# Kernel tuning notes

Hardware: AMD Instinct MI355X
Metric: run time of the kernel (lower is better)

Reference implementation:

```python
import math
import jax, jax.numpy as jnp
import numpy as np

B, T, C, H, V = 2, 512, 768, 12, 50304
HD = C // H
EPS_LN = 1e-5
SINK_ITERS = 6           # MAX_ITER_SINK
N_STEPS = 20             # ceil((1-0)/h_max), h_max=0.05
H_STEP = 1.0 / N_STEPS   # Euler step size h


def layer_norm(x, w, b):
    mu = jnp.mean(x, axis=-1, keepdims=True)
    var = jnp.mean(jnp.square(x - mu), axis=-1, keepdims=True)
    return (x - mu) * jax.lax.rsqrt(var + EPS_LN) * w + b


def sinkhorn_pi(Cmat):
    # log-domain Sinkhorn (eps=1) on cost matrix Cmat [N, T, T]; returns transport plan pi
    n = Cmat.shape[-1]
    log_marg = -jnp.log(jnp.asarray(n, Cmat.dtype))  # log(1/n), uniform marginals
    u = jnp.zeros(Cmat.shape[:-1], Cmat.dtype)
    v = jnp.zeros(Cmat.shape[:-1], Cmat.dtype)
    def M(u, v):
        return -Cmat + u[..., :, None] + v[..., None, :]
    for _ in range(SINK_ITERS):
        u = (log_marg - jax.nn.logsumexp(M(u, v), axis=-1)) + u
        v = (log_marg - jax.nn.logsumexp(M(u, v), axis=-2)) + v
    return jnp.exp(M(u, v))


def block_f(z, t, attn_ln_w, attn_ln_b, c_attn_w, c_attn_b, c_proj_w, c_proj_b,
            mlp_ln_w, mlp_ln_b, c_fc_w, c_fc_b, mlp_proj_w, mlp_proj_b):
    Bz, Tz, Cz = z.shape
    tcol = jnp.full((Bz, Tz, 1), t, z.dtype)
    # attention sub-block: LN over C+1 dims (x concat time)
    x = layer_norm(jnp.concatenate([z, tcol], axis=-1), attn_ln_w, attn_ln_b)
    qkv = x @ c_attn_w + c_attn_b                      # [B,T,3C]
    q, k, v = jnp.split(qkv, 3, axis=-1)
    q = q.reshape(Bz, Tz, H, HD).transpose(0, 2, 1, 3)  # [B,H,T,hd]
    k = k.reshape(Bz, Tz, H, HD).transpose(0, 2, 1, 3)
    v = v.reshape(Bz, Tz, H, HD).transpose(0, 2, 1, 3)
    att = jnp.einsum('bhqd,bhkd->bhqk', q, k) * (1.0 / math.sqrt(HD))
    mask = jnp.tril(jnp.ones((Tz, Tz), dtype=bool))
    att = jax.nn.softmax(jnp.where(mask, att, -jnp.inf), axis=-1)
    pi = sinkhorn_pi(att.reshape(Bz * H, Tz, Tz)) * Tz  # sink(att)[0] * n
    y = jnp.einsum('bhqk,bhkd->bhqd', pi.reshape(Bz, H, Tz, Tz), v)
    y = y.transpose(0, 2, 1, 3).reshape(Bz, Tz, Cz)
    y = y @ c_proj_w + c_proj_b
    # MLP sub-block on LN(concat(attn_out, t))
    ht = layer_norm(jnp.concatenate([y, tcol], axis=-1), mlp_ln_w, mlp_ln_b)
    h1 = jax.nn.gelu(ht @ c_fc_w + c_fc_b, approximate=False)
    return h1 @ mlp_proj_w + mlp_proj_b


def setup_inputs() -> dict:
    key = jax.random.key(0)
    ks = jax.random.split(key, 8)
    s = 0.02
    return {
        'idx': jax.random.randint(ks[0], (B, T), 0, V),
        'wte': s * jax.random.normal(ks[1], (V, C), jnp.float32),
        'wpe': s * jax.random.normal(ks[2], (T, C), jnp.float32),
        'attn_ln_w': jnp.ones((C + 1,), jnp.float32),
        'attn_ln_b': jnp.zeros((C + 1,), jnp.float32),
        'c_attn_w': s * jax.random.normal(ks[3], (C + 1, 3 * C), jnp.float32),
        'c_attn_b': jnp.zeros((3 * C,), jnp.float32),
        'c_proj_w': s * jax.random.normal(ks[4], (C, C), jnp.float32),
        'c_proj_b': jnp.zeros((C,), jnp.float32),
        'mlp_ln_w': jnp.ones((C + 1,), jnp.float32),
        'mlp_ln_b': jnp.zeros((C + 1,), jnp.float32),
        'c_fc_w': s * jax.random.normal(ks[5], (C + 1, 4 * C), jnp.float32),
        'c_fc_b': jnp.zeros((4 * C,), jnp.float32),
        'mlp_proj_w': s * jax.random.normal(ks[6], (4 * C, C), jnp.float32),
        'mlp_proj_b': jnp.zeros((C,), jnp.float32),
        'lnf_w': jnp.ones((C,), jnp.float32),
        'lnf_b': jnp.zeros((C,), jnp.float32),
    }


def reference(idx, wte, wpe, attn_ln_w, attn_ln_b, c_attn_w, c_attn_b, c_proj_w,
              c_proj_b, mlp_ln_w, mlp_ln_b, c_fc_w, c_fc_b, mlp_proj_w, mlp_proj_b,
              lnf_w, lnf_b):
    x = wte[idx] + wpe[jnp.arange(idx.shape[1])]  # [B,T,C]

    def step(carry, _):
        z, t = carry
        dz = block_f(z, t, attn_ln_w, attn_ln_b, c_attn_w, c_attn_b, c_proj_w,
                     c_proj_b, mlp_ln_w, mlp_ln_b, c_fc_w, c_fc_b, mlp_proj_w,
                     mlp_proj_b)
        return (z + H_STEP * dz, t + H_STEP), None

    (x, _), _ = jax.lax.scan(step, (x, jnp.float32(0.0)), None, length=N_STEPS)
    x = layer_norm(x, lnf_w, lnf_b)
    logits = x[:, -1:, :] @ wte.T  # inference path: last position only, tied head
    return logits
```

## Files before the change

### kernel.cpp

```cpp
#include <hip/hip_runtime.h>
#include <hip/hip_bf16.h>
#include <math.h>

typedef unsigned short ushortT;
typedef unsigned int uintT;

#define Bc   2
#define Tc   512
#define Cc   768
#define Hc   12
#define HDc  64
#define Vc   50304
#define BTc  (Bc*Tc)
#define NHc  (Bc*Hc)
#define C3   (3*Cc)
#define C4   (4*Cc)
#define EPS_LN 1e-5f
#define H_STEP 0.05f
#define INVN (1.0f/512.0f)
#define SB   4

typedef float f32x4 __attribute__((ext_vector_type(4)));
typedef __bf16 bf16x8 __attribute__((ext_vector_type(8)));
typedef ushortT us8 __attribute__((ext_vector_type(8)));
typedef uintT u32x4 __attribute__((ext_vector_type(4)));

__device__ __forceinline__ ushortT f2bf(float f) {
    union { float f; unsigned u; } x; x.f = f;
    unsigned r = (x.u + 0x7fffu + ((x.u >> 16) & 1u)) >> 16;
    return (ushortT)r;
}
__device__ __forceinline__ float bf2f(ushortT b) {
    union { unsigned u; float f; } x; x.u = ((unsigned)b) << 16;
    return x.f;
}
__device__ __forceinline__ float bflo(uintT w) {
    union { unsigned u; float f; } x; x.u = w << 16;
    return x.f;
}
__device__ __forceinline__ float bfhi(uintT w) {
    union { unsigned u; float f; } x; x.u = w & 0xffff0000u;
    return x.f;
}

__device__ __forceinline__ void gll16(const ushortT* g, ushortT* l) {
    __builtin_amdgcn_global_load_lds(
        (const __attribute__((address_space(1))) unsigned int*)g,
        (__attribute__((address_space(3))) unsigned int*)l,
        16, 0, 0);
}

__device__ __forceinline__ float waveReduceSumX(float v) {
    for (int o = 32; o; o >>= 1) v += __shfl_xor(v, o);
    return v;
}
__device__ __forceinline__ float blockReduceSum(float v) {
    __shared__ float sm[4];
    for (int o = 32; o; o >>= 1) v += __shfl_down(v, o);
    __syncthreads();
    if ((threadIdx.x & 63) == 0) sm[threadIdx.x >> 6] = v;
    __syncthreads();
    return sm[0] + sm[1] + sm[2] + sm[3];
}

__global__ __launch_bounds__(256)
void wtrans_kernel(const float* __restrict__ W, ushortT* __restrict__ out,
                   int K, int N)
{
    __shared__ float t[32][33];
    int k0 = blockIdx.x * 32, n0 = blockIdx.y * 32;
    int tx = threadIdx.x & 31, ty = threadIdx.x >> 5;
    for (int r = ty; r < 32; r += 8)
        t[r][tx] = W[(size_t)(k0 + r) * N + n0 + tx];
    __syncthreads();
    for (int r = ty; r < 32; r += 8)
        out[(size_t)(n0 + r) * K + k0 + tx] = f2bf(t[tx][r]);
}

__global__ __launch_bounds__(256)
void embed_ln(const int* __restrict__ idx, const float* __restrict__ wte,
              const float* __restrict__ wpe, float* __restrict__ z,
              const float* __restrict__ lnw, const float* __restrict__ lnb,
              ushortT* __restrict__ xlnb, float* __restrict__ xt)
{
    int row = blockIdx.x, tid = threadIdx.x;
    int tok = idx[row];
    float v[3];
#pragma unroll
    for (int q = 0; q < 3; ++q) {
        int c = tid + 256 * q;
        float val = wte[(size_t)tok * Cc + c] + wpe[(size_t)(row & (Tc - 1)) * Cc + c];
        z[(size_t)row * Cc + c] = val;
        v[q] = val;
    }
    float s = blockReduceSum(v[0] + v[1] + v[2]);
    float mu = s / 769.f;
    float d0 = v[0] - mu, d1 = v[1] - mu, d2 = v[2] - mu;
    float ss = blockReduceSum(d0 * d0 + d1 * d1 + d2 * d2);
    float dt = 0.f - mu;
    float var = (ss + dt * dt) / 769.f;
    float rs = rsqrtf(var + EPS_LN);
#pragma unroll
    for (int q = 0; q < 3; ++q) {
        int c = tid + 256 * q;
        xlnb[(size_t)row * Cc + c] = f2bf((v[q] - mu) * rs * lnw[c] + lnb[c]);
    }
    if (tid == 0) xt[row] = dt * rs * lnw[Cc] + lnb[Cc];
}

__global__ __launch_bounds__(256)
void ln_kernel(const float* __restrict__ X, const float* __restrict__ w,
               const float* __restrict__ bb, void* __restrict__ Y,
               float* __restrict__ yt, int hasT, float tval,
               int rowMul, int rowAdd, int obf16)
{
    int orow = blockIdx.x;
    int r = orow * rowMul + rowAdd;
    const float* x = X + (size_t)r * Cc;
    int tid = threadIdx.x;
    float xv[3];
#pragma unroll
    for (int q = 0; q < 3; ++q) xv[q] = x[tid + 256 * q];
    float s = blockReduceSum(xv[0] + xv[1] + xv[2]);
    float cnt = hasT ? 769.f : 768.f;
    float mu = (s + (hasT ? tval : 0.f)) / cnt;
    float d0 = xv[0] - mu, d1 = xv[1] - mu, d2 = xv[2] - mu;
    float ss = blockReduceSum(d0 * d0 + d1 * d1 + d2 * d2);
    float dt = tval - mu;
    float var = (ss + (hasT ? dt * dt : 0.f)) / cnt;
    float rs = rsqrtf(var + EPS_LN);
#pragma unroll
    for (int q = 0; q < 3; ++q) {
        int c = tid + 256 * q;
        float v = (xv[q] - mu) * rs * w[c] + bb[c];
        if (obf16) ((ushortT*)Y)[(size_t)orow * Cc + c] = f2bf(v);
        else       ((float*)Y)[(size_t)orow * Cc + c] = v;
    }
    if (hasT && tid == 0) yt[orow] = dt * rs * w[Cc] + bb[Cc];
}

template <int EPI>
__global__ __launch_bounds__(256)
void gemm_bt(const ushortT* __restrict__ A, int lda,
             const ushortT* __restrict__ Bt, int ldb,
             void* __restrict__ Cm, int ldc, int K,
             const float* __restrict__ bias,
             const float* __restrict__ extraA,
             const float* __restrict__ extraB)
{
    __shared__ __align__(16) ushortT Als[128][32];
    __shared__ __align__(16) ushortT Bls[128][32];
    if (EPI == 4) {
        int koff = blockIdx.z * K;
        A += koff; Bt += koff;
    }
    int tid = threadIdx.x;
    int lane = tid & 63, wid = tid >> 6;
    int wm = wid >> 1, wn = wid & 1;
    int m0 = blockIdx.y * 128, n0 = blockIdx.x * 128;
    f32x4 acc[4][4];
    const f32x4 fz = {0.f, 0.f, 0.f, 0.f};
#pragma unroll
    for (int i = 0; i < 4; ++i)
#pragma unroll
        for (int j = 0; j < 4; ++j) acc[i][j] = fz;

    for (int k0 = 0; k0 < K; k0 += 32) {
#pragma unroll
        for (int is = 0; is < 2; ++is) {
            int ch = is * 256 + tid;
            int m = ch >> 2, kc = ch & 3;
            gll16(A + (size_t)(m0 + m) * lda + k0 + kc * 8, &Als[0][0] + ch * 8);
            gll16(Bt + (size_t)(n0 + m) * ldb + k0 + kc * 8, &Bls[0][0] + ch * 8);
        }
        __syncthreads();
        bf16x8 af[4], bfv[4];
#pragma unroll
        for (int i = 0; i < 4; ++i) {
            int row = wm * 64 + i * 16 + (lane & 15);
            af[i] = *(const bf16x8*)&Als[row][(lane >> 4) * 8];
            int col = wn * 64 + i * 16 + (lane & 15);
            bfv[i] = *(const bf16x8*)&Bls[col][(lane >> 4) * 8];
        }
#pragma unroll
        for (int i = 0; i < 4; ++i)
#pragma unroll
            for (int j = 0; j < 4; ++j)
                acc[i][j] = __builtin_amdgcn_mfma_f32_16x16x32_bf16(af[i], bfv[j], acc[i][j], 0, 0, 0);
        __syncthreads();
    }
#pragma unroll
    for (int i = 0; i < 4; ++i) {
#pragma unroll
        for (int j = 0; j < 4; ++j) {
#pragma unroll
            for (int r = 0; r < 4; ++r) {
                int row = m0 + wm * 64 + i * 16 + (lane >> 4) * 4 + r;
                int col = n0 + wn * 64 + j * 16 + (lane & 15);
                float v = acc[i][j][r];
                if (extraA) v += extraA[row] * extraB[col];
                if (bias) v += bias[col];
                size_t oi = (size_t)row * ldc + col;
                if (EPI == 0) {
                    ((ushortT*)Cm)[oi] = f2bf(v);
                } else if (EPI == 1) {
                    v = 0.5f * v * (1.f + erff(v * 0.70710678118654752440f));
                    ((ushortT*)Cm)[oi] = f2bf(v);
                } else if (EPI == 3) {
                    ((float*)Cm)[oi] = v;
                } else if (EPI == 4) {
                    ((float*)Cm)[(size_t)blockIdx.z * ((size_t)BTc * Cc) + oi] = v;
                }
            }
        }
    }
}

__global__ __launch_bounds__(512)
void sinkfused(const ushortT* __restrict__ qkvb, ushortT* __restrict__ E,
               float* __restrict__ avec, ushortT* __restrict__ vTs,
               float* __restrict__ partials, unsigned* __restrict__ ctr,
               unsigned barBase)
{
    int gb = blockIdx.x;
    int n = gb >> 2, r = gb & 3;
    int row0 = r * 128;
    int b = n / Hc, h = n - b * Hc;
    int tid = threadIdx.x;
    int l = tid & 63, w = tid >> 6;
    __shared__ __align__(16) ushortT Els[128][Tc];
    __shared__ __align__(16) ushortT Kls[128][64];
    __shared__ float a_s[128];
    __shared__ float b_s[Tc];
    ushortT* Eg = E + (size_t)n * Tc * Tc;
    const f32x4 fz = {0.f, 0.f, 0.f, 0.f};

    int qrow = b * Tc + row0 + w * 16 + (l & 15);
    const ushortT* qp = qkvb + (size_t)qrow * C3 + h * HDc + (l >> 4) * 8;
    bf16x8 aq0 = *(const bf16x8*)(qp);
    bf16x8 aq1 = *(const bf16x8*)(qp + 32);

    int kcmax = r + 1;
    f32x4 acc[32];
#pragma unroll
    for (int j = 0; j < 32; ++j) acc[j] = fz;

#pragma unroll
    for (int kc = 0; kc < 4; ++kc) {
        if (kc < kcmax) {
            {
                int ch = tid;
                int row = ch >> 3, c16 = (ch & 7) ^ (row & 7);
                gll16(qkvb + (size_t)(b * Tc + kc * 128 + row) * C3 + Cc + h * HDc + c16 * 8,
                      &Kls[0][0] + ch * 8);
                ch = tid + 512;
                row = ch >> 3; c16 = (ch & 7) ^ (row & 7);
                gll16(qkvb + (size_t)(b * Tc + kc * 128 + row) * C3 + Cc + h * HDc + c16 * 8,
                      &Kls[0][0] + ch * 8);
            }
            __syncthreads();
#pragma unroll
            for (int jj = 0; jj < 8; ++jj) {
                int krow = jj * 16 + (l & 15);
                int c16a = (l >> 4);
                int c16b = 4 + (l >> 4);
                bf16x8 bk0 = *(const bf16x8*)(&Kls[0][0] + ((size_t)krow * 8 + (c16a ^ (krow & 7))) * 8);
                bf16x8 bk1 = *(const bf16x8*)(&Kls[0][0] + ((size_t)krow * 8 + (c16b ^ (krow & 7))) * 8);
                acc[kc * 8 + jj] = __builtin_amdgcn_mfma_f32_16x16x32_bf16(aq0, bk0, acc[kc * 8 + jj], 0, 0, 0);
                acc[kc * 8 + jj] = __builtin_amdgcn_mfma_f32_16x16x32_bf16(aq1, bk1, acc[kc * 8 + jj], 0, 0, 0);
            }
            __syncthreads();
        }
    }

    int nvalid = kcmax * 8;
    int colbase = (l & 15);
    int rowa[4];
#pragma unroll
    for (int e = 0; e < 4; ++e) rowa[e] = row0 + w * 16 + (l >> 4) * 4 + e;

    float mx[4] = {-INFINITY, -INFINITY, -INFINITY, -INFINITY};
#pragma unroll
    for (int j = 0; j < 32; ++j) {
        if (j < nvalid) {
            int col = j * 16 + colbase;
#pragma unroll
            for (int e = 0; e < 4; ++e)
                if (col <= rowa[e]) mx[e] = fmaxf(mx[e], acc[j][e] * 0.125f);
        }
    }
#pragma unroll
    for (int e = 0; e < 4; ++e)
        for (int o = 1; o < 16; o <<= 1) mx[e] = fmaxf(mx[e], __shfl_xor(mx[e], o));

    float se[4] = {0.f, 0.f, 0.f, 0.f};
#pragma unroll
    for (int j = 0; j < 32; ++j) {
        if (j < nvalid) {
            int col = j * 16 + colbase;
#pragma unroll
            for (int e = 0; e < 4; ++e) {
                float exv = (col <= rowa[e]) ? __expf(acc[j][e] * 0.125f - mx[e]) : 0.f;
                acc[j][e] = exv;
                se[e] += exv;
            }
        }
    }
#pragma unroll
    for (int e = 0; e < 4; ++e)
        for (int o = 1; o < 16; o <<= 1) se[e] += __shfl_xor(se[e], o);
    float inv[4];
#pragma unroll
    for (int e = 0; e < 4; ++e) inv[e] = 1.f / se[e];

    float rsum[4] = {0.f, 0.f, 0.f, 0.f};
#pragma unroll
    for (int j = 0; j < 32; ++j) {
        if (j < nvalid) {
            int col = j * 16 + colbase;
#pragma unroll
            for (int e = 0; e < 4; ++e) {
                float Ee = __expf(-(acc[j][e] * inv[e]));
                rsum[e] += Ee;
                Els[w * 16 + (l >> 4) * 4 + e][col] = f2bf(Ee);
            }
        }
    }
#pragma unroll
    for (int e = 0; e < 4; ++e) {
        for (int o = 1; o < 16; o <<= 1) rsum[e] += __shfl_xor(rsum[e], o);
        if ((l & 15) == 0)
            a_s[w * 16 + (l >> 4) * 4 + e] = INVN / (rsum[e] + (float)(Tc - nvalid * 16));
    }
    {
        int tailc = 64 - kcmax * 16;
        if (tailc > 0) {
            us8 ones8;
#pragma unroll
            for (int e = 0; e < 8; ++e) ones8[e] = 0x3F80;
            for (int idx2 = l; idx2 < 16 * tailc; idx2 += 64) {
                int rr = idx2 / tailc, cc = idx2 - rr * tailc;
                *(us8*)&Els[w * 16 + rr][(kcmax * 16 + cc) * 8] = ones8;
            }
        }
    }
    __syncthreads();

#pragma unroll
    for (int ii = 0; ii < 16; ++ii) {
        int flat = ii * 512 + tid;
        int rr = flat >> 6, c = flat & 63;
        *(us8*)(Eg + (((size_t)(row0 + rr)) << 9) + c * 8) = *(const us8*)&Els[rr][c * 8];
    }

    float* mypart = partials + (size_t)(n * SB + r) * Tc;
    const float* hpart = partials + (size_t)n * SB * Tc;
    unsigned* myctr = ctr + n * 16;

#pragma unroll 1
    for (int p = 0; p < 11; ++p) {
        if ((p & 1) == 0) {
            int j = tid;
            float accs = 0.f;
#pragma unroll 1
            for (int i = 0; i < 128; i += 8) {
                float part = 0.f;
#pragma unroll
                for (int k = 0; k < 8; ++k)
                    part += bf2f(Els[i + k][j]) * a_s[i + k];
                accs += part;
            }
            __hip_atomic_store(&mypart[j], accs, __ATOMIC_RELAXED, __HIP_MEMORY_SCOPE_AGENT);
            __syncthreads();
            if (tid == 0) {
                __threadfence();
                atomicAdd(myctr, 1u);
                unsigned tgt = barBase + (unsigned)(p / 2 + 1) * SB;
                while (__hip_atomic_load(myctr, __ATOMIC_ACQUIRE, __HIP_MEMORY_SCOPE_AGENT) < tgt)
                    __builtin_amdgcn_s_sleep(2);
            }
            __syncthreads();
            float s0 = __hip_atomic_load(&hpart[j], __ATOMIC_RELAXED, __HIP_MEMORY_SCOPE_AGENT);
            float s1 = __hip_atomic_load(&hpart[Tc + j], __ATOMIC_RELAXED, __HIP_MEMORY_SCOPE_AGENT);
            float s2 = __hip_atomic_load(&hpart[2 * Tc + j], __ATOMIC_RELAXED, __HIP_MEMORY_SCOPE_AGENT);
            float s3 = __hip_atomic_load(&hpart[3 * Tc + j], __ATOMIC_RELAXED, __HIP_MEMORY_SCOPE_AGENT);
            b_s[j] = INVN / (s0 + s1 + s2 + s3);
            __syncthreads();
        } else {
            f32x4 b0 = *(const f32x4*)&b_s[l * 8];
            f32x4 b1 = *(const f32x4*)&b_s[l * 8 + 4];
            float breg[8] = {b0[0], b0[1], b0[2], b0[3], b1[0], b1[1], b1[2], b1[3]};
#pragma unroll 1
            for (int k = 0; k < 16; k += 4) {
                int r0 = w * 16 + k;
                u32x4 q0 = *(const u32x4*)(&Els[r0 + 0][l * 8]);
                u32x4 q1 = *(const u32x4*)(&Els[r0 + 1][l * 8]);
                u32x4 q2 = *(const u32x4*)(&Els[r0 + 2][l * 8]);
                u32x4 q3 = *(const u32x4*)(&Els[r0 + 3][l * 8]);
                float s0 = 0.f, s1 = 0.f, s2 = 0.f, s3 = 0.f;
#pragma unroll
                for (int c = 0; c < 4; ++c) {
                    s0 += bflo(q0[c]) * breg[2 * c] + bfhi(q0[c]) * breg[2 * c + 1];
                    s1 += bflo(q1[c]) * breg[2 * c] + bfhi(q1[c]) * breg[2 * c + 1];
                    s2 += bflo(q2[c]) * breg[2 * c] + bfhi(q2[c]) * breg[2 * c + 1];
                    s3 += bflo(q3[c]) * breg[2 * c] + bfhi(q3[c]) * breg[2 * c + 1];
                }
                s0 = waveReduceSumX(s0);
                s1 = waveReduceSumX(s1);
                s2 = waveReduceSumX(s2);
                s3 = waveReduceSumX(s3);
                if (l == 0) {
                    a_s[r0 + 0] = INVN / s0;
                    a_s[r0 + 1] = INVN / s1;
                    a_s[r0 + 2] = INVN / s2;
                    a_s[r0 + 3] = INVN / s3;
                }
            }
            __syncthreads();
        }
    }

    {
        f32x4 b0 = *(const f32x4*)&b_s[l * 8];
        f32x4 b1 = *(const f32x4*)&b_s[l * 8 + 4];
        float breg[8] = {b0[0], b0[1], b0[2], b0[3], b1[0], b1[1], b1[2], b1[3]};
#pragma unroll
        for (int dd = 0; dd < 2; ++dd) {
            int d = r * 16 + w * 2 + dd;
            const ushortT* vs = qkvb + (size_t)(b * Tc) * C3 + 2 * Cc + h * HDc + d;
            us8 o;
#pragma unroll
            for (int e = 0; e < 8; ++e) {
                float vv = bf2f(vs[(size_t)(l * 8 + e) * C3]);
                o[e] = f2bf(vv * 512.f * breg[e]);
            }
            *(us8*)(vTs + ((size_t)n * HDc + d) * Tc + l * 8) = o;
        }
        if (tid < 128) avec[n * Tc + row0 + tid] = a_s[tid];
    }
}

__global__ __launch_bounds__(256)
void piv_mfma(const ushortT* __restrict__ E, const ushortT* __restrict__ vTs,
              const float* __restrict__ avec, ushortT* __restrict__ y)
{
    int n = blockIdx.y; int b = n / Hc, h = n - b * Hc;
    int m0 = blockIdx.x * 128;
    const ushortT* Ap = E + (size_t)n * Tc * Tc;
    const ushortT* Bv = vTs + (size_t)n * HDc * Tc;
    __shared__ __align__(16) ushortT Als[128][32];
    __shared__ __align__(16) ushortT Bls[64][32];
    int tid = threadIdx.x;
    int lane = tid & 63, wid = tid >> 6;
    int wm = wid >> 1, wn = wid & 1;
    f32x4 acc[4][2];
    const f32x4 fz = {0.f, 0.f, 0.f, 0.f};
#pragma unroll
    for (int i = 0; i < 4; ++i)
#pragma unroll
        for (int j = 0; j < 2; ++j) acc[i][j] = fz;

    for (int k0 = 0; k0 < Tc; k0 += 32) {
#pragma unroll
        for (int is = 0; is < 2; ++is) {
            int ch = is * 256 + tid;
            int m = ch >> 2, kc = ch & 3;
            gll16(Ap + (size_t)(m0 + m) * Tc + k0 + kc * 8, &Als[0][0] + ch * 8);
        }
        {
            int ch = tid;
            int d = ch >> 2, kc = ch & 3;
            gll16(Bv + (size_t)d * Tc + k0 + kc * 8, &Bls[0][0] + ch * 8);
        }
        __syncthreads();
        bf16x8 af[4], bfv[2];
#pragma unroll
        for (int i = 0; i < 4; ++i) {
            int row = wm * 64 + i * 16 + (lane & 15);
            af[i] = *(const bf16x8*)&Als[row][(lane >> 4) * 8];
        }
#pragma unroll
        for (int j = 0; j < 2; ++j) {
            int col = wn * 32 + j * 16 + (lane & 15);
            bfv[j] = *(const bf16x8*)&Bls[col][(lane >> 4) * 8];
        }
#pragma unroll
        for (int i = 0; i < 4; ++i)
#pragma unroll
            for (int j = 0; j < 2; ++j)
                acc[i][j] = __builtin_amdgcn_mfma_f32_16x16x32_bf16(af[i], bfv[j], acc[i][j], 0, 0, 0);
        __syncthreads();
    }
#pragma unroll
    for (int i = 0; i < 4; ++i)
#pragma unroll
        for (int j = 0; j < 2; ++j)
#pragma unroll
            for (int r = 0; r < 4; ++r) {
                int rIn = m0 + wm * 64 + i * 16 + (lane >> 4) * 4 + r;
                float a_r = avec[n * Tc + rIn];
                int row = b * Tc + rIn;
                int col = h * HDc + wn * 32 + j * 16 + (lane & 15);
                y[(size_t)row * Cc + col] = f2bf(acc[i][j][r] * a_r);
            }
}

__global__ __launch_bounds__(256)
void reduce_ln(const float* __restrict__ parts, const float* __restrict__ bias,
               float* __restrict__ z, const float* __restrict__ lnw,
               const float* __restrict__ lnb, ushortT* __restrict__ xlnb,
               float* __restrict__ xt, float tval)
{
    int row = blockIdx.x, tid = threadIdx.x;
    const size_t CS = (size_t)BTc * Cc;
    float v[3];
#pragma unroll
    for (int q = 0; q < 3; ++q) {
        int c = tid + 256 * q;
        size_t idx = (size_t)row * Cc + c;
        float s = parts[idx] + parts[CS + idx] + parts[2 * CS + idx]
                + parts[3 * CS + idx] + bias[c];
        v[q] = z[idx] + H_STEP * s;
        z[idx] = v[q];
    }
    float s = blockReduceSum(v[0] + v[1] + v[2]);
    float mu = (s + tval) / 769.f;
    float d0 = v[0] - mu, d1 = v[1] - mu, d2 = v[2] - mu;
    float ss = blockReduceSum(d0 * d0 + d1 * d1 + d2 * d2);
    float dt = tval - mu;
    float var = (ss + dt * dt) / 769.f;
    float rs = rsqrtf(var + EPS_LN);
#pragma unroll
    for (int q = 0; q < 3; ++q) {
        int c = tid + 256 * q;
        xlnb[(size_t)row * Cc + c] = f2bf((v[q] - mu) * rs * lnw[c] + lnb[c]);
    }
    if (tid == 0) xt[row] = dt * rs * lnw[Cc] + lnb[Cc];
}

__global__ __launch_bounds__(256)
void logits_kernel(const float* __restrict__ xf, const float* __restrict__ wte,
                   float* __restrict__ out)
{
    __shared__ __align__(16) float xs[2 * Cc];
    int tid = threadIdx.x;
    for (int i = tid; i < 384; i += 256)
        ((f32x4*)xs)[i] = ((const f32x4*)xf)[i];
    __syncthreads();
    int w = tid >> 6, lane = tid & 63;
    int vrow = blockIdx.x * 4 + w;
    const f32x4* wr = (const f32x4*)(wte + (size_t)vrow * Cc);
    const f32x4* x0 = (const f32x4*)xs;
    const f32x4* x1 = (const f32x4*)(xs + Cc);
    float a0 = 0.f, a1 = 0.f;
#pragma unroll
    for (int it = 0; it < 3; ++it) {
        int k4 = it * 64 + lane;
        f32x4 wv = wr[k4];
        f32x4 p = x0[k4], q = x1[k4];
        a0 += wv[0] * p[0] + wv[1] * p[1] + wv[2] * p[2] + wv[3] * p[3];
        a1 += wv[0] * q[0] + wv[1] * q[1] + wv[2] * q[2] + wv[3] * q[3];
    }
    for (int o = 32; o; o >>= 1) {
        a0 += __shfl_down(a0, o);
        a1 += __shfl_down(a1, o);
    }
    if (lane == 0) {
        out[vrow] = a0;
        out[Vc + vrow] = a1;
    }
}

extern "C" void kernel_launch(void* const* d_in, const int* in_sizes, int n_in,
                              void* d_out, int out_size, void* d_ws, size_t ws_size,
                              hipStream_t stream)
{
    const int*   idx        = (const int*)  d_in[0];
    const float* wte        = (const float*)d_in[1];
    const float* wpe        = (const float*)d_in[2];
    const float* attn_ln_w  = (const float*)d_in[3];
    const float* attn_ln_b  = (const float*)d_in[4];
    const float* c_attn_w   = (const float*)d_in[5];
    const float* c_attn_b   = (const float*)d_in[6];
    const float* c_proj_w   = (const float*)d_in[7];
    const float* c_proj_b   = (const float*)d_in[8];
    const float* mlp_ln_w   = (const float*)d_in[9];
    const float* mlp_ln_b   = (const float*)d_in[10];
    const float* c_fc_w     = (const float*)d_in[11];
    const float* c_fc_b     = (const float*)d_in[12];
    const float* mlp_proj_w = (const float*)d_in[13];
    const float* mlp_proj_b = (const float*)d_in[14];
    const float* lnf_w      = (const float*)d_in[15];
    const float* lnf_b      = (const float*)d_in[16];
    float* out = (float*)d_out;

    char* base = (char*)d_ws;
    size_t off = 0;
    auto alloc = [&](size_t bytes) -> void* {
        void* p = base + off;
        off = (off + bytes + 255) & ~(size_t)255;
        return p;
    };
    float*   z     = (float*)  alloc((size_t)BTc * Cc * 4);
    float*   parts = (float*)  alloc((size_t)4 * BTc * Cc * 4);
    ushortT* E     = (ushortT*)alloc((size_t)NHc * Tc * Tc * 2);
    ushortT* qkvb  = (ushortT*)alloc((size_t)BTc * C3 * 2);
    ushortT* xlnb  = (ushortT*)alloc((size_t)BTc * Cc * 2);
    ushortT* y     = (ushortT*)alloc((size_t)BTc * Cc * 2);
    ushortT* h1    = (ushortT*)alloc((size_t)BTc * C4 * 2);
    ushortT* vTs   = (ushortT*)alloc((size_t)NHc * HDc * Tc * 2);
    float*   ao    = (float*)  alloc((size_t)BTc * Cc * 4);
    float*   xt    = (float*)  alloc(BTc * 4);
    float*   avec  = (float*)  alloc(NHc * Tc * 4);
    float*   partv = (float*)  alloc((size_t)NHc * SB * Tc * 4);
    unsigned* ctr  = (unsigned*)alloc(NHc * 16 * 4);
    float*   xf    = (float*)  alloc(2 * Cc * 4);
    ushortT* WqkvT = (ushortT*)alloc((size_t)C3 * Cc * 2);
    ushortT* WprojT= (ushortT*)alloc((size_t)Cc * Cc * 2);
    ushortT* WfcT  = (ushortT*)alloc((size_t)C4 * Cc * 2);
    ushortT* WmlpT = (ushortT*)alloc((size_t)Cc * C4 * 2);

    hipMemsetAsync(ctr, 0, NHc * 16 * 4, stream);
    embed_ln<<<BTc, 256, 0, stream>>>(idx, wte, wpe, z, attn_ln_w, attn_ln_b, xlnb, xt);
    wtrans_kernel<<<dim3(Cc / 32, C3 / 32), 256, 0, stream>>>(c_attn_w,   WqkvT,  Cc, C3);
    wtrans_kernel<<<dim3(Cc / 32, Cc / 32), 256, 0, stream>>>(c_proj_w,   WprojT, Cc, Cc);
    wtrans_kernel<<<dim3(Cc / 32, C4 / 32), 256, 0, stream>>>(c_fc_w,     WfcT,   Cc, C4);
    wtrans_kernel<<<dim3(C4 / 32, Cc / 32), 256, 0, stream>>>(mlp_proj_w, WmlpT,  C4, Cc);

    float t = 0.f;
    for (int step = 0; step < 20; ++step) {
        gemm_bt<0><<<dim3(C3 / 128, BTc / 128), 256, 0, stream>>>(
            xlnb, Cc, WqkvT, Cc, qkvb, C3, Cc,
            c_attn_b, xt, c_attn_w + (size_t)Cc * C3);
        sinkfused<<<NHc * SB, 512, 0, stream>>>(
            qkvb, E, avec, vTs, partv, ctr, (unsigned)(step * 6 * SB));
        piv_mfma<<<dim3(Tc / 128, NHc), 256, 0, stream>>>(E, vTs, avec, y);
        gemm_bt<3><<<dim3(Cc / 128, BTc / 128), 256, 0, stream>>>(
            y, Cc, WprojT, Cc, ao, Cc, Cc,
            c_proj_b, nullptr, nullptr);
        ln_kernel<<<BTc, 256, 0, stream>>>(ao, mlp_ln_w, mlp_ln_b, xlnb, xt, 1, t, 1, 0, 1);
        gemm_bt<1><<<dim3(C4 / 128, BTc / 128), 256, 0, stream>>>(
            xlnb, Cc, WfcT, Cc, h1, C4, Cc,
            c_fc_b, xt, c_fc_w + (size_t)Cc * C4);
        gemm_bt<4><<<dim3(Cc / 128, BTc / 128, 4), 256, 0, stream>>>(
            h1, C4, WmlpT, C4, parts, Cc, C4 / 4,
            nullptr, nullptr, nullptr);
        t += H_STEP;
        reduce_ln<<<BTc, 256, 0, stream>>>(parts, mlp_proj_b, z,
                                           attn_ln_w, attn_ln_b, xlnb, xt, t);
    }

    ln_kernel<<<2, 256, 0, stream>>>(z, lnf_w, lnf_b, xf, nullptr, 0, 0.f, Tc, Tc - 1, 0);
    logits_kernel<<<Vc / 4, 256, 0, stream>>>(xf, wte, out);
}
```

Measured before the change: 4.192 ms.

## Fuse pi@V product into Sinkhorn kernel, dropping global E matrix and piv kernel

The Sinkhorn kernel now computes the final pi·V product directly from its shared-memory exp tile, using MFMA over V chunks scaled by the column factors. This removes the global write of the bf16 E matrix, the separate vTs/avec buffers and the piv_mfma launch, saving global traffic and one kernel per step. The Els tile gets padding to ease LDS bank conflicts. In exchange, only 96 blocks do the PV work, and the V transpose goes through LDS with strided stores.

```diff
diff --git a/kernel.cpp b/kernel.cpp
--- a/kernel.cpp
+++ b/kernel.cpp
@@ -19,6 +19,7 @@
 #define H_STEP 0.05f
 #define INVN (1.0f/512.0f)
 #define SB   4
+#define ELP  (Tc + 8)
 
 typedef float f32x4 __attribute__((ext_vector_type(4)));
 typedef __bf16 bf16x8 __attribute__((ext_vector_type(8)));
@@ -217,8 +218,7 @@
 }
 
 __global__ __launch_bounds__(512)
-void sinkfused(const ushortT* __restrict__ qkvb, ushortT* __restrict__ E,
-               float* __restrict__ avec, ushortT* __restrict__ vTs,
+void sinkfused(const ushortT* __restrict__ qkvb, ushortT* __restrict__ y,
                float* __restrict__ partials, unsigned* __restrict__ ctr,
                unsigned barBase)
 {
@@ -228,11 +228,10 @@
     int b = n / Hc, h = n - b * Hc;
     int tid = threadIdx.x;
     int l = tid & 63, w = tid >> 6;
-    __shared__ __align__(16) ushortT Els[128][Tc];
-    __shared__ __align__(16) ushortT Kls[128][64];
+    __shared__ __align__(16) ushortT Els[128][ELP];
+    __shared__ __align__(16) ushortT Kshare[128 * 64];
     __shared__ float a_s[128];
     __shared__ float b_s[Tc];
-    ushortT* Eg = E + (size_t)n * Tc * Tc;
     const f32x4 fz = {0.f, 0.f, 0.f, 0.f};
 
     int qrow = b * Tc + row0 + w * 16 + (l & 15);
@@ -252,11 +251,11 @@
                 int ch = tid;
                 int row = ch >> 3, c16 = (ch & 7) ^ (row & 7);
                 gll16(qkvb + (size_t)(b * Tc + kc * 128 + row) * C3 + Cc + h * HDc + c16 * 8,
-                      &Kls[0][0] + ch * 8);
+                      Kshare + ch * 8);
                 ch = tid + 512;
                 row = ch >> 3; c16 = (ch & 7) ^ (row & 7);
                 gll16(qkvb + (size_t)(b * Tc + kc * 128 + row) * C3 + Cc + h * HDc + c16 * 8,
-                      &Kls[0][0] + ch * 8);
+                      Kshare + ch * 8);
             }
             __syncthreads();
 #pragma unroll
@@ -264,8 +263,8 @@
                 int krow = jj * 16 + (l & 15);
                 int c16a = (l >> 4);
                 int c16b = 4 + (l >> 4);
-                bf16x8 bk0 = *(const bf16x8*)(&Kls[0][0] + ((size_t)krow * 8 + (c16a ^ (krow & 7))) * 8);
-                bf16x8 bk1 = *(const bf16x8*)(&Kls[0][0] + ((size_t)krow * 8 + (c16b ^ (krow & 7))) * 8);
+                bf16x8 bk0 = *(const bf16x8*)(Kshare + ((size_t)krow * 8 + (c16a ^ (krow & 7))) * 8);
+                bf16x8 bk1 = *(const bf16x8*)(Kshare + ((size_t)krow * 8 + (c16b ^ (krow & 7))) * 8);
                 acc[kc * 8 + jj] = __builtin_amdgcn_mfma_f32_16x16x32_bf16(aq0, bk0, acc[kc * 8 + jj], 0, 0, 0);
                 acc[kc * 8 + jj] = __builtin_amdgcn_mfma_f32_16x16x32_bf16(aq1, bk1, acc[kc * 8 + jj], 0, 0, 0);
             }
@@ -345,13 +344,6 @@
         }
     }
     __syncthreads();
-
-#pragma unroll
-    for (int ii = 0; ii < 16; ++ii) {
-        int flat = ii * 512 + tid;
-        int rr = flat >> 6, c = flat & 63;
-        *(us8*)(Eg + (((size_t)(row0 + rr)) << 9) + c * 8) = *(const us8*)&Els[rr][c * 8];
-    }
 
     float* mypart = partials + (size_t)(n * SB + r) * Tc;
     const float* hpart = partials + (size_t)n * SB * Tc;
@@ -421,88 +413,56 @@
     }
 
     {
-        f32x4 b0 = *(const f32x4*)&b_s[l * 8];
-        f32x4 b1 = *(const f32x4*)&b_s[l * 8 + 4];
-        float breg[8] = {b0[0], b0[1], b0[2], b0[3], b1[0], b1[1], b1[2], b1[3]};
-#pragma unroll
-        for (int dd = 0; dd < 2; ++dd) {
-            int d = r * 16 + w * 2 + dd;
-            const ushortT* vs = qkvb + (size_t)(b * Tc) * C3 + 2 * Cc + h * HDc + d;
-            us8 o;
-#pragma unroll
-            for (int e = 0; e < 8; ++e) {
-                float vv = bf2f(vs[(size_t)(l * 8 + e) * C3]);
-                o[e] = f2bf(vv * 512.f * breg[e]);
-            }
-            *(us8*)(vTs + ((size_t)n * HDc + d) * Tc + l * 8) = o;
-        }
-        if (tid < 128) avec[n * Tc + row0 + tid] = a_s[tid];
-    }
-}
-
-__global__ __launch_bounds__(256)
-void piv_mfma(const ushortT* __restrict__ E, const ushortT* __restrict__ vTs,
-              const float* __restrict__ avec, ushortT* __restrict__ y)
-{
-    int n = blockIdx.y; int b = n / Hc, h = n - b * Hc;
-    int m0 = blockIdx.x * 128;
-    const ushortT* Ap = E + (size_t)n * Tc * Tc;
-    const ushortT* Bv = vTs + (size_t)n * HDc * Tc;
-    __shared__ __align__(16) ushortT Als[128][32];
-    __shared__ __align__(16) ushortT Bls[64][32];
-    int tid = threadIdx.x;
-    int lane = tid & 63, wid = tid >> 6;
-    int wm = wid >> 1, wn = wid & 1;
-    f32x4 acc[4][2];
-    const f32x4 fz = {0.f, 0.f, 0.f, 0.f};
-#pragma unroll
-    for (int i = 0; i < 4; ++i)
-#pragma unroll
-        for (int j = 0; j < 2; ++j) acc[i][j] = fz;
-
-    for (int k0 = 0; k0 < Tc; k0 += 32) {
-#pragma unroll
-        for (int is = 0; is < 2; ++is) {
-            int ch = is * 256 + tid;
-            int m = ch >> 2, kc = ch & 3;
-            gll16(Ap + (size_t)(m0 + m) * Tc + k0 + kc * 8, &Als[0][0] + ch * 8);
-        }
-        {
-            int ch = tid;
-            int d = ch >> 2, kc = ch & 3;
-            gll16(Bv + (size_t)d * Tc + k0 + kc * 8, &Bls[0][0] + ch * 8);
-        }
-        __syncthreads();
-        bf16x8 af[4], bfv[2];
-#pragma unroll
-        for (int i = 0; i < 4; ++i) {
-            int row = wm * 64 + i * 16 + (lane & 15);
-            af[i] = *(const bf16x8*)&Als[row][(lane >> 4) * 8];
-        }
-#pragma unroll
-        for (int j = 0; j < 2; ++j) {
-            int col = wn * 32 + j * 16 + (lane & 15);
-            bfv[j] = *(const bf16x8*)&Bls[col][(lane >> 4) * 8];
-        }
-#pragma unroll
-        for (int i = 0; i < 4; ++i)
+        ushortT* Kls2 = Kshare;
+        int wm = w >> 1, wn = w & 1;
+        f32x4 acc2[2][2];
+#pragma unroll
+        for (int i = 0; i < 2; ++i)
+#pragma unroll
+            for (int j = 0; j < 2; ++j) acc2[i][j] = fz;
+        const ushortT* vbase = qkvb + (size_t)(b * Tc) * C3 + 2 * Cc + h * HDc;
+
+#pragma unroll 1
+        for (int k0 = 0; k0 < Tc; k0 += 64) {
+            {
+                int tt = tid >> 3, dblk = tid & 7;
+                us8 vv = *(const us8*)(vbase + (size_t)(k0 + tt) * C3 + dblk * 8);
+                float bs = 512.f * b_s[k0 + tt];
+#pragma unroll
+                for (int e = 0; e < 8; ++e)
+                    Kls2[(dblk * 8 + e) * 72 + tt] = f2bf(bf2f(vv[e]) * bs);
+            }
+            __syncthreads();
+#pragma unroll
+            for (int kk = 0; kk < 64; kk += 32) {
+                bf16x8 af[2], bv[2];
+#pragma unroll
+                for (int i = 0; i < 2; ++i)
+                    af[i] = *(const bf16x8*)&Els[wm * 32 + i * 16 + (l & 15)][k0 + kk + (l >> 4) * 8];
+#pragma unroll
+                for (int j = 0; j < 2; ++j)
+                    bv[j] = *(const bf16x8*)(Kls2 + (size_t)(wn * 32 + j * 16 + (l & 15)) * 72 + kk + (l >> 4) * 8);
+#pragma unroll
+                for (int i = 0; i < 2; ++i)
+#pragma unroll
+                    for (int j = 0; j < 2; ++j)
+                        acc2[i][j] = __builtin_amdgcn_mfma_f32_16x16x32_bf16(af[i], bv[j], acc2[i][j], 0, 0, 0);
+            }
+            __syncthreads();
+        }
+#pragma unroll
+        for (int i = 0; i < 2; ++i)
 #pragma unroll
             for (int j = 0; j < 2; ++j)
-                acc[i][j] = __builtin_amdgcn_mfma_f32_16x16x32_bf16(af[i], bfv[j], acc[i][j], 0, 0, 0);
-        __syncthreads();
-    }
-#pragma unroll
-    for (int i = 0; i < 4; ++i)
-#pragma unroll
-        for (int j = 0; j < 2; ++j)
-#pragma unroll
-            for (int r = 0; r < 4; ++r) {
-                int rIn = m0 + wm * 64 + i * 16 + (lane >> 4) * 4 + r;
-                float a_r = avec[n * Tc + rIn];
-                int row = b * Tc + rIn;
-                int col = h * HDc + wn * 32 + j * 16 + (lane & 15);
-                y[(size_t)row * Cc + col] = f2bf(acc[i][j][r] * a_r);
-            }
+#pragma unroll
+                for (int rr = 0; rr < 4; ++rr) {
+                    int lrow = wm * 32 + i * 16 + (l >> 4) * 4 + rr;
+                    float a_r = a_s[lrow];
+                    int grow = b * Tc + row0 + lrow;
+                    int gcol = h * HDc + wn * 32 + j * 16 + (l & 15);
+                    y[(size_t)grow * Cc + gcol] = f2bf(acc2[i][j][rr] * a_r);
+                }
+    }
 }
 
 __global__ __launch_bounds__(256)
@@ -603,15 +563,12 @@
     };
     float*   z     = (float*)  alloc((size_t)BTc * Cc * 4);
     float*   parts = (float*)  alloc((size_t)4 * BTc * Cc * 4);
-    ushortT* E     = (ushortT*)alloc((size_t)NHc * Tc * Tc * 2);
     ushortT* qkvb  = (ushortT*)alloc((size_t)BTc * C3 * 2);
     ushortT* xlnb  = (ushortT*)alloc((size_t)BTc * Cc * 2);
     ushortT* y     = (ushortT*)alloc((size_t)BTc * Cc * 2);
     ushortT* h1    = (ushortT*)alloc((size_t)BTc * C4 * 2);
-    ushortT* vTs   = (ushortT*)alloc((size_t)NHc * HDc * Tc * 2);
     float*   ao    = (float*)  alloc((size_t)BTc * Cc * 4);
     float*   xt    = (float*)  alloc(BTc * 4);
-    float*   avec  = (float*)  alloc(NHc * Tc * 4);
     float*   partv = (float*)  alloc((size_t)NHc * SB * Tc * 4);
     unsigned* ctr  = (unsigned*)alloc(NHc * 16 * 4);
     float*   xf    = (float*)  alloc(2 * Cc * 4);
@@ -633,8 +590,7 @@
             xlnb, Cc, WqkvT, Cc, qkvb, C3, Cc,
             c_attn_b, xt, c_attn_w + (size_t)Cc * C3);
         sinkfused<<<NHc * SB, 512, 0, stream>>>(
-            qkvb, E, avec, vTs, partv, ctr, (unsigned)(step * 6 * SB));
-        piv_mfma<<<dim3(Tc / 128, NHc), 256, 0, stream>>>(E, vTs, avec, y);
+            qkvb, y, partv, ctr, (unsigned)(step * 6 * SB));
         gemm_bt<3><<<dim3(Cc / 128, BTc / 128), 256, 0, stream>>>(
             y, Cc, WprojT, Cc, ao, Cc, Cc,
             c_proj_b, nullptr, nullptr);
```

After: 4.089 ms. 1.03x faster.
